# Performance work log

Hardware: AMD Instinct MI355X
Metric: run time of the kernel (lower is better)

Reference implementation:

```python
import jax, jax.numpy as jnp
import numpy as np

H = 256          # hidden_size
N_NODE = 50000   # item vocab
E_FULL = 500000  # full-graph edges
B = 1024         # sessions per batch
NODES_PER = 12   # session nodes per graph (contiguous, equal sections)
N = B * NODES_PER


def setup_inputs() -> dict:
    key = jax.random.key(0)
    ks = jax.random.split(key, 20)
    stdv = 1.0 / np.sqrt(H)
    u = lambda k, shape: jax.random.uniform(k, shape, jnp.float32, -stdv, stdv)
    return dict(
        x=jax.random.randint(ks[0], (N, 1), 1, N_NODE + 1, dtype=jnp.int32),  # 1-based item ids
        batch=jnp.repeat(jnp.arange(B, dtype=jnp.int32), NODES_PER),          # sorted graph ids
        edge_index=jax.random.randint(ks[1], (2, N), 0, N, dtype=jnp.int32),
        full_graph=jax.random.randint(ks[2], (2, E_FULL), 0, N_NODE, dtype=jnp.int32),
        emb=u(ks[3], (N_NODE, H)),
        ggnn_W=u(ks[4], (H, H)),
        gru_Wih=u(ks[5], (3 * H, H)),
        gru_Whh=u(ks[6], (3 * H, H)),
        gru_bih=u(ks[7], (3 * H,)),
        gru_bhh=u(ks[8], (3 * H,)),
        W1_w=u(ks[9], (H, H)), W1_b=u(ks[10], (H,)),
        W2_w=u(ks[11], (H, H)), W2_b=u(ks[12], (H,)),
        q_w=u(ks[13], (1, H)), q_b=u(ks[14], (1,)),
        W3_w=u(ks[15], (H, 2 * H)), W3_b=u(ks[16], (H,)),
    )


def _forward(x, batch, edge_index, full_graph, emb, ggnn_W, gru_Wih, gru_Whh,
             gru_bih, gru_bhh, W1_w, W1_b, W2_w, W2_b, q_w, q_b, W3_w, W3_b):
    # --- GatedGraphConv (num_layers=1) over the full item graph ---
    src, dst = full_graph[0], full_graph[1]
    m = emb @ ggnn_W                                      # [n_node, H]
    agg = jax.ops.segment_sum(m[src], dst, num_segments=N_NODE)  # sum aggregation
    # GRUCell(agg, emb)
    gi = agg @ gru_Wih.T + gru_bih                        # [n_node, 3H]
    gh = emb @ gru_Whh.T + gru_bhh
    i_r, i_z, i_n = jnp.split(gi, 3, axis=1)
    h_r, h_z, h_n = jnp.split(gh, 3, axis=1)
    r = jax.nn.sigmoid(i_r + h_r)
    z = jax.nn.sigmoid(i_z + h_z)
    n = jnp.tanh(i_n + r * h_n)
    hidden_all = (1.0 - z) * n + z * emb                  # [n_node, H]

    # gather session nodes (x is 1-based), relu
    h2 = jax.nn.relu(hidden_all[x[:, 0] - 1])             # [N, H]

    # --- Embedding2Score: segment attention readout ---
    sections = jax.ops.segment_sum(jnp.ones_like(batch), batch, num_segments=B)
    last_idx = jnp.cumsum(sections) - 1                   # last node of each session
    v_n = h2[last_idx]                                    # [B, H]
    v_n_rep = v_n[batch]                                  # [N, H]
    gate = jax.nn.sigmoid(v_n_rep @ W1_w.T + W1_b + h2 @ W2_w.T + W2_b)
    alpha = gate @ q_w.T + q_b                            # [N, 1]
    s_g = jax.ops.segment_sum(alpha * h2, batch, num_segments=B)  # [B, H]
    s_h = jnp.concatenate([v_n, s_g], axis=1) @ W3_w.T + W3_b     # [B, H]
    scores = s_h @ emb.T                                  # [B, n_node]
    return scores, h2


def reference(x, batch, edge_index, full_graph, emb, ggnn_W, gru_Wih, gru_Whh,
              gru_bih, gru_bhh, W1_w, W1_b, W2_w, W2_b, q_w, q_b, W3_w, W3_b):
    scores, h2 = _forward(x, batch, edge_index, full_graph, emb, ggnn_W,
                          gru_Wih, gru_Whh, gru_bih, gru_bhh,
                          W1_w, W1_b, W2_w, W2_b, q_w, q_b, W3_w, W3_b)
    return scores, h2, edge_index
```

## Files before the change

kernel.cpp:

```cpp
#include <hip/hip_runtime.h>
#include <hip/hip_bf16.h>
#include <stdint.h>

#define HDIM 256
#define NNODE 50000
#define EFULL 500000
#define BSESS 1024
#define NPER 12
#define NROWS 12288
#define CAP 96

typedef __attribute__((ext_vector_type(8))) short bf16x8;
typedef __attribute__((ext_vector_type(4))) float f32x4;
typedef __attribute__((ext_vector_type(4))) unsigned short u16x4;

__device__ __forceinline__ float bf2f(unsigned short v) {
  union { unsigned u; float f; } x; x.u = ((unsigned)v) << 16; return x.f;
}
__device__ __forceinline__ unsigned short f2bf(float f) {
  union { float f; unsigned u; } x; x.f = f;
  unsigned r = x.u + 0x7fff + ((x.u >> 16) & 1);
  return (unsigned short)(r >> 16);
}

#define CV_EMB   12800000
#define CV_GW    65536
#define CV_WIH   196608
#define CV_WHH   196608
#define CV_W1    65536
#define CV_W2    65536
#define CV_W3    131072
#define CV_BIAS  2304
#define CV_WSUM  (CV_EMB + CV_GW + CV_WIH + CV_WHH + CV_W1 + CV_W2 + CV_W3 + CV_BIAS)
#define CV_TOTAL (CV_WSUM + NNODE + 2 * NROWS)
__global__ void k_conv(const float* __restrict__ emb, const float* __restrict__ gw,
                       const float* __restrict__ wih, const float* __restrict__ whh,
                       const float* __restrict__ w1, const float* __restrict__ w2,
                       const float* __restrict__ w3,
                       const float* __restrict__ bih, const float* __restrict__ bhh,
                       const float* __restrict__ w1b, const float* __restrict__ w2b,
                       const float* __restrict__ w3b,
                       unsigned short* __restrict__ embB, unsigned short* __restrict__ gwB,
                       unsigned short* __restrict__ wihB, unsigned short* __restrict__ whhB,
                       unsigned short* __restrict__ w1B, unsigned short* __restrict__ w2B,
                       unsigned short* __restrict__ w3B, unsigned short* __restrict__ biasB,
                       int* __restrict__ map,
                       const int* __restrict__ eidx, float* __restrict__ out_e) {
  long idx = (long)blockIdx.x * 256 + threadIdx.x;
  if (idx < CV_EMB) { embB[idx] = f2bf(emb[idx]); return; }
  idx -= CV_EMB;
  if (idx < CV_GW)  { gwB[idx] = f2bf(gw[idx]); return; }
  idx -= CV_GW;
  if (idx < CV_WIH) { wihB[idx] = f2bf(wih[idx]); return; }
  idx -= CV_WIH;
  if (idx < CV_WHH) { whhB[idx] = f2bf(whh[idx]); return; }
  idx -= CV_WHH;
  if (idx < CV_W1)  { w1B[idx] = f2bf(w1[idx]); return; }
  idx -= CV_W1;
  if (idx < CV_W2)  { w2B[idx] = f2bf(w2[idx]); return; }
  idx -= CV_W2;
  if (idx < CV_W3)  { w3B[idx] = f2bf(w3[idx]); return; }
  idx -= CV_W3;
  if (idx < CV_BIAS) {
    if (idx < 768)        { biasB[idx] = f2bf(bih[idx]); return; }
    if (idx < 1536)       { biasB[idx] = f2bf(bhh[idx - 768]); return; }
    if (idx < 1792)       { biasB[idx] = f2bf(w1b[idx - 1536]); return; }
    if (idx < 2048)       { biasB[idx] = f2bf(w2b[idx - 1792]); return; }
    biasB[idx] = f2bf(w3b[idx - 2048]); return;
  }
  idx -= CV_BIAS;
  if (idx < NNODE) { map[idx] = -1; return; }
  idx -= NNODE;
  if (idx < 2 * NROWS) out_e[idx] = (float)eidx[idx];
}

__global__ void k_set_map(const int* __restrict__ x, int* __restrict__ m, int* __restrict__ cnt) {
  int i = blockIdx.x * 256 + threadIdx.x;
  if (i < NROWS) { atomicMax(&m[x[i] - 1], i); cnt[i] = 0; }
}

__global__ void k_bin(const int* __restrict__ fg, const int* __restrict__ map,
                      int* __restrict__ cnt, int* __restrict__ lists) {
  int e = blockIdx.x * 256 + threadIdx.x;
  if (e >= EFULL) return;
  int cid = map[fg[EFULL + e]];
  if (cid < 0) return;
  int pos = atomicAdd(&cnt[cid], 1);
  if (pos < CAP) lists[cid * CAP + pos] = fg[e];
}

#define PREP_COPY_BLKS 1284
#define PREP_AGG_BASE  (12 + PREP_COPY_BLKS)
__global__ __launch_bounds__(256) void k_prep(
    const unsigned short* __restrict__ WihB, const unsigned short* __restrict__ gwB,
    const unsigned short* __restrict__ WhhB,
    const float* __restrict__ bih, const float* __restrict__ bhh,
    unsigned short* __restrict__ Bbig2, unsigned short* __restrict__ bias2,
    const int* __restrict__ x, const int* __restrict__ map,
    const int* __restrict__ cnt, const int* __restrict__ lists,
    const float* __restrict__ emb, unsigned short* __restrict__ Acat) {
  __shared__ __align__(16) unsigned short As[128 * 32];
  __shared__ __align__(16) unsigned short Bs[128 * 32];
  if (blockIdx.x < 12) {
    const int bx = blockIdx.x % 6, by = blockIdx.x / 6;
    const int tid = threadIdx.x;
    const int wid = tid >> 6, lane = tid & 63;
    const int quad = lane >> 4, l15 = lane & 15;
    const int m0 = bx * 128, n0 = by * 128;
    const int wm = (wid & 1) * 64, wn = (wid >> 1) * 64;
    f32x4 acc[4][4] = {};
    const int lrow = tid >> 2;
    const int lcol = (tid & 3) * 8;
    const size_t ar0 = (size_t)(m0 + lrow) * HDIM + lcol;
    const size_t ar1 = (size_t)(m0 + lrow + 64) * HDIM + lcol;
    const size_t br0 = (size_t)(n0 + lrow) * HDIM + lcol;
    const size_t br1 = (size_t)(n0 + lrow + 64) * HDIM + lcol;
    const int ak = quad * 8;
    for (int k0 = 0; k0 < HDIM; k0 += 32) {
      *(float4*)&As[(size_t)tid * 8]        = *(const float4*)&WihB[ar0 + k0];
      *(float4*)&As[2048 + (size_t)tid * 8] = *(const float4*)&WihB[ar1 + k0];
      *(float4*)&Bs[(size_t)tid * 8]        = *(const float4*)&gwB[br0 + k0];
      *(float4*)&Bs[2048 + (size_t)tid * 8] = *(const float4*)&gwB[br1 + k0];
      __syncthreads();
      bf16x8 af[4], bfv[4];
#pragma unroll
      for (int mi = 0; mi < 4; mi++) af[mi] = *(const bf16x8*)&As[(wm + mi * 16 + l15) * 32 + ak];
#pragma unroll
      for (int ni = 0; ni < 4; ni++) bfv[ni] = *(const bf16x8*)&Bs[(wn + ni * 16 + l15) * 32 + ak];
#pragma unroll
      for (int mi = 0; mi < 4; mi++)
#pragma unroll
        for (int ni = 0; ni < 4; ni++)
          acc[mi][ni] = __builtin_amdgcn_mfma_f32_16x16x32_bf16(af[mi], bfv[ni], acc[mi][ni], 0, 0, 0);
      __syncthreads();
    }
#pragma unroll
    for (int mi = 0; mi < 4; mi++) {
      const int gr0 = m0 + wm + mi * 16 + quad * 4;
#pragma unroll
      for (int ni = 0; ni < 4; ni++) {
        const int gc = n0 + wn + ni * 16 + l15;
#pragma unroll
        for (int r = 0; r < 4; r++) {
          const int gr = gr0 + r;
          const int g = gr >> 8, c = gr & 255;
          const int jp = ((c >> 4) << 6) + (g << 4) + (c & 15);
          Bbig2[(size_t)jp * 512 + gc] = f2bf(acc[mi][ni][r]);
        }
      }
    }
    return;
  }
  if (blockIdx.x < PREP_AGG_BASE) {
    int idx = (blockIdx.x - 12) * 256 + threadIdx.x;
    if (idx < 262144) {
      int jp = idx >> 8, kk = idx & 255;
      int g = (jp >> 4) & 3, q = jp >> 6, t = jp & 15, c = q * 16 + t;
      unsigned short v = 0;
      if (g < 2)       v = WhhB[(size_t)(g * 256 + c) * HDIM + kk];
      else if (g == 3) v = WhhB[(size_t)(512 + c) * HDIM + kk];
      Bbig2[(size_t)jp * 512 + 256 + kk] = v;
      return;
    }
    idx -= 262144;
    if (idx < 65536) {
      int c = idx >> 8, k = idx & 255;
      int jp = ((c >> 4) << 6) + 48 + (c & 15);
      Bbig2[(size_t)jp * 512 + k] = 0;
      return;
    }
    idx -= 65536;
    if (idx < 1024) {
      int q = idx >> 6, g = (idx >> 4) & 3, t = idx & 15, c = q * 16 + t;
      float bv;
      if (g < 2)       bv = bih[g * 256 + c] + bhh[g * 256 + c];
      else if (g == 2) bv = bih[512 + c];
      else             bv = bhh[512 + c];
      bias2[idx] = f2bf(bv);
    }
    return;
  }
  int i = (blockIdx.x - PREP_AGG_BASE) * 4 + (threadIdx.x >> 6);
  int lane = threadIdx.x & 63;
  int node = x[i] - 1;
  int cid = map[node];
  int n = cnt[cid];
  if (n > CAP) n = CAP;
  const int* lp = lists + (size_t)cid * CAP;
  float sx = 0.f, sy = 0.f, sz = 0.f, sw = 0.f;
  int j = 0;
  for (; j + 4 <= n; j += 4) {
    int s0 = lp[j], s1 = lp[j + 1], s2 = lp[j + 2], s3 = lp[j + 3];
    float4 v0 = *(const float4*)(emb + (size_t)s0 * HDIM + lane * 4);
    float4 v1 = *(const float4*)(emb + (size_t)s1 * HDIM + lane * 4);
    float4 v2 = *(const float4*)(emb + (size_t)s2 * HDIM + lane * 4);
    float4 v3 = *(const float4*)(emb + (size_t)s3 * HDIM + lane * 4);
    sx += v0.x + v1.x + v2.x + v3.x;
    sy += v0.y + v1.y + v2.y + v3.y;
    sz += v0.z + v1.z + v2.z + v3.z;
    sw += v0.w + v1.w + v2.w + v3.w;
  }
  for (; j < n; j++) {
    int s0 = lp[j];
    float4 v0 = *(const float4*)(emb + (size_t)s0 * HDIM + lane * 4);
    sx += v0.x; sy += v0.y; sz += v0.z; sw += v0.w;
  }
  u16x4 o; o.x = f2bf(sx); o.y = f2bf(sy); o.z = f2bf(sz); o.w = f2bf(sw);
  *(u16x4*)(Acat + (size_t)i * 512 + lane * 4) = o;
  float4 v = *(const float4*)(emb + (size_t)node * HDIM + lane * 4);
  u16x4 o2; o2.x = f2bf(v.x); o2.y = f2bf(v.y); o2.z = f2bf(v.z); o2.w = f2bf(v.w);
  *(u16x4*)(Acat + (size_t)i * 512 + 256 + lane * 4) = o2;
}

template <bool OUT_BF16>
__device__ __forceinline__ void gemm128_body(
    unsigned short* As, unsigned short* Bs,
    const unsigned short* __restrict__ A, int lda,
    const unsigned short* __restrict__ Bm, int ldb,
    const unsigned short* __restrict__ bias,
    void* __restrict__ C, int ldc, int M, int N, int K, int bx, int by) {
  const int tid = threadIdx.x;
  const int wid = tid >> 6, lane = tid & 63;
  const int quad = lane >> 4, l15 = lane & 15;
  const int m0 = bx * 128, n0 = by * 128;
  const int wm = (wid & 1) * 64, wn = (wid >> 1) * 64;
  f32x4 acc[4][4] = {};
  const int lrow = tid >> 2;
  const int lcol = (tid & 3) * 8;
  const size_t ar0 = (size_t)min(m0 + lrow, M - 1) * lda + lcol;
  const size_t ar1 = (size_t)min(m0 + lrow + 64, M - 1) * lda + lcol;
  const size_t br0 = (size_t)min(n0 + lrow, N - 1) * ldb + lcol;
  const size_t br1 = (size_t)min(n0 + lrow + 64, N - 1) * ldb + lcol;
  const int ak = quad * 8;
  for (int k0 = 0; k0 < K; k0 += 32) {
    *(float4*)&As[(size_t)tid * 8]        = *(const float4*)&A[ar0 + k0];
    *(float4*)&As[2048 + (size_t)tid * 8] = *(const float4*)&A[ar1 + k0];
    *(float4*)&Bs[(size_t)tid * 8]        = *(const float4*)&Bm[br0 + k0];
    *(float4*)&Bs[2048 + (size_t)tid * 8] = *(const float4*)&Bm[br1 + k0];
    __syncthreads();
    bf16x8 af[4], bfv[4];
#pragma unroll
    for (int mi = 0; mi < 4; mi++) af[mi] = *(const bf16x8*)&As[(wm + mi * 16 + l15) * 32 + ak];
#pragma unroll
    for (int ni = 0; ni < 4; ni++) bfv[ni] = *(const bf16x8*)&Bs[(wn + ni * 16 + l15) * 32 + ak];
#pragma unroll
    for (int mi = 0; mi < 4; mi++)
#pragma unroll
      for (int ni = 0; ni < 4; ni++)
        acc[mi][ni] = __builtin_amdgcn_mfma_f32_16x16x32_bf16(af[mi], bfv[ni], acc[mi][ni], 0, 0, 0);
    __syncthreads();
  }
#pragma unroll
  for (int mi = 0; mi < 4; mi++) {
    const int gr0 = m0 + wm + mi * 16 + quad * 4;
#pragma unroll
    for (int ni = 0; ni < 4; ni++) {
      const int gc = n0 + wn + ni * 16 + l15;
      if (gc >= N) continue;
      const float bv = bias ? bf2f(bias[gc]) : 0.f;
#pragma unroll
      for (int r = 0; r < 4; r++) {
        const int gr = gr0 + r;
        if (gr < M) {
          const float v = acc[mi][ni][r] + bv;
          if (OUT_BF16) ((unsigned short*)C)[(size_t)gr * ldc + gc] = f2bf(v);
          else          ((float*)C)[(size_t)gr * ldc + gc] = v;
        }
      }
    }
  }
}

__global__ __launch_bounds__(256) void k_t12(
    const unsigned short* __restrict__ h2b, const unsigned short* __restrict__ W2, const unsigned short* __restrict__ b2,
    unsigned short* __restrict__ t2,
    const unsigned short* __restrict__ vnB, const unsigned short* __restrict__ W1, const unsigned short* __restrict__ b1,
    unsigned short* __restrict__ t1) {
  __shared__ __align__(16) unsigned short As[128 * 32];
  __shared__ __align__(16) unsigned short Bs[128 * 32];
  if (blockIdx.x < 96)
    gemm128_body<true>(As, Bs, h2b, HDIM, W2, HDIM, b2, t2, HDIM, NROWS, HDIM, HDIM, blockIdx.x, blockIdx.y);
  else
    gemm128_body<true>(As, Bs, vnB, HDIM, W1, HDIM, b1, t1, HDIM, BSESS, HDIM, HDIM, blockIdx.x - 96, blockIdx.y);
}

__global__ __launch_bounds__(512) void k_ggru(
    const unsigned short* __restrict__ Acat,
    const unsigned short* __restrict__ Bbig2,
    const unsigned short* __restrict__ bias2,
    unsigned short* __restrict__ h2b, float* __restrict__ h2out,
    unsigned short* __restrict__ vnB) {
  __shared__ __align__(16) unsigned short As[256 * 32];
  __shared__ __align__(16) unsigned short Bs[128 * 32];
  const int tid = threadIdx.x;
  const int wid = tid >> 6, lane = tid & 63;
  const int quad = lane >> 4, l15 = lane & 15;
  const int m0 = blockIdx.x * 256, n0 = blockIdx.y * 128;
  const int wm = (wid & 3) * 64, wn = (wid >> 2) * 64;
  f32x4 acc[4][4] = {};
  const int lrow = tid >> 2;
  const int lcol = (tid & 3) * 8;
  const size_t ar0 = (size_t)(m0 + lrow) * 512 + lcol;
  const size_t ar1 = (size_t)(m0 + lrow + 128) * 512 + lcol;
  const size_t br0 = (size_t)(n0 + lrow) * 512 + lcol;
  const int ak = quad * 8;
  for (int k0 = 0; k0 < 512; k0 += 32) {
    *(float4*)&As[(size_t)lrow * 32 + lcol]         = *(const float4*)&Acat[ar0 + k0];
    *(float4*)&As[(size_t)(lrow + 128) * 32 + lcol] = *(const float4*)&Acat[ar1 + k0];
    *(float4*)&Bs[(size_t)lrow * 32 + lcol]         = *(const float4*)&Bbig2[br0 + k0];
    __syncthreads();
    bf16x8 af[4], bfv[4];
#pragma unroll
    for (int mi = 0; mi < 4; mi++) af[mi] = *(const bf16x8*)&As[(wm + mi * 16 + l15) * 32 + ak];
#pragma unroll
    for (int g = 0; g < 4; g++) bfv[g] = *(const bf16x8*)&Bs[(wn + g * 16 + l15) * 32 + ak];
#pragma unroll
    for (int mi = 0; mi < 4; mi++)
#pragma unroll
      for (int g = 0; g < 4; g++)
        acc[mi][g] = __builtin_amdgcn_mfma_f32_16x16x32_bf16(af[mi], bfv[g], acc[mi][g], 0, 0, 0);
    __syncthreads();
  }
  const int ch = ((n0 + wn) >> 2) + l15;
  const float b0 = bf2f(bias2[(n0 + wn) + 0 * 16 + l15]);
  const float b1 = bf2f(bias2[(n0 + wn) + 1 * 16 + l15]);
  const float b2 = bf2f(bias2[(n0 + wn) + 2 * 16 + l15]);
  const float b3 = bf2f(bias2[(n0 + wn) + 3 * 16 + l15]);
#pragma unroll
  for (int mi = 0; mi < 4; mi++) {
    const int gr0 = m0 + wm + mi * 16 + quad * 4;
#pragma unroll
    for (int r = 0; r < 4; r++) {
      const int gr = gr0 + r;
      float rs = acc[mi][0][r] + b0;
      float zs = acc[mi][1][r] + b1;
      float inn = acc[mi][2][r] + b2;
      float hn = acc[mi][3][r] + b3;
      float rr = 1.f / (1.f + expf(-rs));
      float zz = 1.f / (1.f + expf(-zs));
      float nn = tanhf(inn + rr * hn);
      float e = bf2f(Acat[(size_t)gr * 512 + 256 + ch]);
      float h = fmaxf((1.f - zz) * nn + zz * e, 0.f);
      unsigned short hb = f2bf(h);
      h2b[(size_t)gr * HDIM + ch] = hb;
      h2out[(size_t)gr * HDIM + ch] = h;
      if (gr % NPER == NPER - 1) vnB[(size_t)(gr / NPER) * HDIM + ch] = hb;
    }
  }
}

__global__ __launch_bounds__(256) void k_attn2(
    const unsigned short* __restrict__ t1, const unsigned short* __restrict__ t2,
    const unsigned short* __restrict__ h2b,
    const float* __restrict__ qw, const float* __restrict__ qb,
    const unsigned short* __restrict__ W3, const unsigned short* __restrict__ b3,
    unsigned short* __restrict__ shb) {
  __shared__ float al[NPER];
  __shared__ float sh[512];
  const int b = blockIdx.x;
  const int w = threadIdx.x >> 6, lane = threadIdx.x & 63;
  u16x4 a = *(const u16x4*)(t1 + (size_t)b * HDIM + lane * 4);
  float4 q = *(const float4*)(qw + lane * 4);
  float ax = bf2f(a.x), ay = bf2f(a.y), az = bf2f(a.z), aw = bf2f(a.w);
#pragma unroll
  for (int i = 0; i < 3; i++) {
    int j = w * 3 + i;
    u16x4 c = *(const u16x4*)(t2 + ((size_t)b * NPER + j) * HDIM + lane * 4);
    float p = 0.f;
    p += q.x / (1.f + expf(-(ax + bf2f(c.x))));
    p += q.y / (1.f + expf(-(ay + bf2f(c.y))));
    p += q.z / (1.f + expf(-(az + bf2f(c.z))));
    p += q.w / (1.f + expf(-(aw + bf2f(c.w))));
#pragma unroll
    for (int off = 32; off > 0; off >>= 1) p += __shfl_down(p, off);
    if (lane == 0) al[j] = p + qb[0];
  }
  const int c = threadIdx.x;
  sh[c] = bf2f(h2b[((size_t)b * NPER + (NPER - 1)) * HDIM + c]);
  __syncthreads();
  float s = 0.f;
#pragma unroll
  for (int j = 0; j < NPER; j++)
    s += al[j] * bf2f(h2b[((size_t)b * NPER + j) * HDIM + c]);
  sh[256 + c] = s;
  __syncthreads();
  const unsigned short* wrow = W3 + (size_t)c * 512;
  float acc = bf2f(b3[c]);
#pragma unroll 8
  for (int k = 0; k < 512; k += 8) {
    bf16x8 wv = *(const bf16x8*)&wrow[k];
    acc += bf2f((unsigned short)wv[0]) * sh[k + 0];
    acc += bf2f((unsigned short)wv[1]) * sh[k + 1];
    acc += bf2f((unsigned short)wv[2]) * sh[k + 2];
    acc += bf2f((unsigned short)wv[3]) * sh[k + 3];
    acc += bf2f((unsigned short)wv[4]) * sh[k + 4];
    acc += bf2f((unsigned short)wv[5]) * sh[k + 5];
    acc += bf2f((unsigned short)wv[6]) * sh[k + 6];
    acc += bf2f((unsigned short)wv[7]) * sh[k + 7];
  }
  shb[(size_t)b * HDIM + c] = f2bf(acc);
}

template <bool OUT_BF16>
__global__ __launch_bounds__(512) void k_gemm_nt2(
    const unsigned short* __restrict__ A, int lda,
    const unsigned short* __restrict__ Bm, int ldb,
    const unsigned short* __restrict__ bias,
    void* __restrict__ C, int ldc, int M, int N, int K) {
  __shared__ __align__(16) unsigned short As[256 * 32];
  __shared__ __align__(16) unsigned short Bs[128 * 32];
  const int tid = threadIdx.x;
  const int wid = tid >> 6, lane = tid & 63;
  const int quad = lane >> 4, l15 = lane & 15;
  const int m0 = blockIdx.x * 256, n0 = blockIdx.y * 128;
  const int wm = (wid & 3) * 64, wn = (wid >> 2) * 64;
  f32x4 acc[4][4] = {};
  const int lrow = tid >> 2;
  const int lcol = (tid & 3) * 8;
  const size_t ar0 = (size_t)min(m0 + lrow, M - 1) * lda + lcol;
  const size_t ar1 = (size_t)min(m0 + lrow + 128, M - 1) * lda + lcol;
  const size_t br0 = (size_t)min(n0 + lrow, N - 1) * ldb + lcol;
  const int ak = quad * 8;
  for (int k0 = 0; k0 < K; k0 += 32) {
    *(float4*)&As[(size_t)lrow * 32 + lcol]         = *(const float4*)&A[ar0 + k0];
    *(float4*)&As[(size_t)(lrow + 128) * 32 + lcol] = *(const float4*)&A[ar1 + k0];
    *(float4*)&Bs[(size_t)lrow * 32 + lcol]         = *(const float4*)&Bm[br0 + k0];
    __syncthreads();
    bf16x8 af[4], bfv[4];
#pragma unroll
    for (int mi = 0; mi < 4; mi++) af[mi] = *(const bf16x8*)&As[(wm + mi * 16 + l15) * 32 + ak];
#pragma unroll
    for (int ni = 0; ni < 4; ni++) bfv[ni] = *(const bf16x8*)&Bs[(wn + ni * 16 + l15) * 32 + ak];
#pragma unroll
    for (int mi = 0; mi < 4; mi++)
#pragma unroll
      for (int ni = 0; ni < 4; ni++)
        acc[mi][ni] = __builtin_amdgcn_mfma_f32_16x16x32_bf16(af[mi], bfv[ni], acc[mi][ni], 0, 0, 0);
    __syncthreads();
  }
#pragma unroll
  for (int mi = 0; mi < 4; mi++) {
    const int gr0 = m0 + wm + mi * 16 + quad * 4;
#pragma unroll
    for (int ni = 0; ni < 4; ni++) {
      const int gc = n0 + wn + ni * 16 + l15;
      if (gc >= N) continue;
      const float bv = bias ? bf2f(bias[gc]) : 0.f;
#pragma unroll
      for (int r = 0; r < 4; r++) {
        const int gr = gr0 + r;
        if (gr < M) {
          const float v = acc[mi][ni][r] + bv;
          if (OUT_BF16) ((unsigned short*)C)[(size_t)gr * ldc + gc] = f2bf(v);
          else          ((float*)C)[(size_t)gr * ldc + gc] = v;
        }
      }
    }
  }
}

extern "C" void kernel_launch(void* const* d_in, const int* in_sizes, int n_in,
                              void* d_out, int out_size, void* d_ws, size_t ws_size,
                              hipStream_t stream) {
  const int* x     = (const int*)d_in[0];
  const int* batch = (const int*)d_in[1];
  const int* eidx  = (const int*)d_in[2];
  const int* fg    = (const int*)d_in[3];
  const float* emb   = (const float*)d_in[4];
  const float* ggnnW = (const float*)d_in[5];
  const float* Wih   = (const float*)d_in[6];
  const float* Whh   = (const float*)d_in[7];
  const float* bih   = (const float*)d_in[8];
  const float* bhh   = (const float*)d_in[9];
  const float* W1w   = (const float*)d_in[10];
  const float* W1b   = (const float*)d_in[11];
  const float* W2w   = (const float*)d_in[12];
  const float* W2b   = (const float*)d_in[13];
  const float* qw    = (const float*)d_in[14];
  const float* qb    = (const float*)d_in[15];
  const float* W3w   = (const float*)d_in[16];
  const float* W3b   = (const float*)d_in[17];
  (void)batch;

  char* w = (char*)d_ws;
  size_t off = 0;
  auto alloc = [&](size_t bytes) { char* p = w + off; off += (bytes + 511) & ~(size_t)511; return p; };
  int*            map   = (int*)alloc((size_t)NNODE * 4);
  int*            cnt   = (int*)alloc((size_t)NROWS * 4);
  int*            lists = (int*)alloc((size_t)NROWS * CAP * 4);
  unsigned short* Acat  = (unsigned short*)alloc((size_t)NROWS * 512 * 2);
  unsigned short* embB  = (unsigned short*)alloc((size_t)NNODE * HDIM * 2);
  unsigned short* gwB   = (unsigned short*)alloc((size_t)CV_GW * 2);
  unsigned short* WihB  = (unsigned short*)alloc((size_t)CV_WIH * 2);
  unsigned short* WhhB  = (unsigned short*)alloc((size_t)CV_WHH * 2);
  unsigned short* W1wB  = (unsigned short*)alloc((size_t)CV_W1 * 2);
  unsigned short* W2wB  = (unsigned short*)alloc((size_t)CV_W2 * 2);
  unsigned short* W3wB  = (unsigned short*)alloc((size_t)CV_W3 * 2);
  unsigned short* biasB = (unsigned short*)alloc((size_t)CV_BIAS * 2);
  unsigned short* Bbig2 = (unsigned short*)alloc((size_t)1024 * 512 * 2);
  unsigned short* bias2 = (unsigned short*)alloc((size_t)1024 * 2);
  unsigned short* h2b   = (unsigned short*)alloc((size_t)NROWS * HDIM * 2);
  unsigned short* vnB   = (unsigned short*)alloc((size_t)BSESS * HDIM * 2);
  unsigned short* t1    = (unsigned short*)alloc((size_t)BSESS * HDIM * 2);
  unsigned short* t2    = (unsigned short*)alloc((size_t)NROWS * HDIM * 2);
  unsigned short* shb   = (unsigned short*)alloc((size_t)BSESS * HDIM * 2);
  if (off > ws_size) return;

  float* out_scores = (float*)d_out;
  float* out_h2     = out_scores + (size_t)BSESS * NNODE;
  float* out_e      = out_h2 + (size_t)NROWS * HDIM;

  dim3 blk(256);
  k_conv   <<<(CV_TOTAL + 255) / 256, blk, 0, stream>>>(emb, ggnnW, Wih, Whh, W1w, W2w, W3w,
               bih, bhh, W1b, W2b, W3b, embB, gwB, WihB, WhhB, W1wB, W2wB, W3wB, biasB,
               map, eidx, out_e);
  k_set_map<<<(NROWS + 255) / 256, blk, 0, stream>>>(x, map, cnt);
  k_bin    <<<(EFULL + 255) / 256, blk, 0, stream>>>(fg, map, cnt, lists);
  k_prep   <<<PREP_AGG_BASE + NROWS / 4, blk, 0, stream>>>(WihB, gwB, WhhB, bih, bhh, Bbig2, bias2,
               x, map, cnt, lists, emb, Acat);
  k_ggru   <<<dim3(48, 8), dim3(512), 0, stream>>>(Acat, Bbig2, bias2, h2b, out_h2, vnB);
  k_t12    <<<dim3(104, 2), blk, 0, stream>>>(h2b, W2wB, biasB + 1792, t2, vnB, W1wB, biasB + 1536, t1);
  k_attn2  <<<BSESS, blk, 0, stream>>>(t1, t2, h2b, qw, qb, W3wB, biasB + 2048, shb);
  k_gemm_nt2<false><<<dim3(4, 391), dim3(512), 0, stream>>>(shb, HDIM, embB, HDIM, nullptr, out_scores, NNODE, BSESS, NNODE, HDIM);
}
```

Measured before the change: 476.5 us.

## Fuse emb bf16 conversion into scores GEMM and shrink GGRU tiles

Removes the separate full-table fp32-to-bf16 conversion of the embedding matrix (12.8M elements) from k_conv and converts emb tiles on the fly inside a specialized scores GEMM kernel. This drops one write and one read of a bf16 copy of emb, but the scores kernel now reads fp32 emb (twice the bytes per tile) and converts it redundantly across the 4 row-block tiles. Separately, the GGRU GEMM moves from 256x128 tiles with 512 threads to 128x128 tiles with 256 threads, doubling the block count for better occupancy and balance.

```diff
diff --git a/kernel.cpp b/kernel.cpp
--- a/kernel.cpp
+++ b/kernel.cpp
@@ -23,7 +23,6 @@
   return (unsigned short)(r >> 16);
 }
 
-#define CV_EMB   12800000
 #define CV_GW    65536
 #define CV_WIH   196608
 #define CV_WHH   196608
@@ -31,24 +30,22 @@
 #define CV_W2    65536
 #define CV_W3    131072
 #define CV_BIAS  2304
-#define CV_WSUM  (CV_EMB + CV_GW + CV_WIH + CV_WHH + CV_W1 + CV_W2 + CV_W3 + CV_BIAS)
+#define CV_WSUM  (CV_GW + CV_WIH + CV_WHH + CV_W1 + CV_W2 + CV_W3 + CV_BIAS)
 #define CV_TOTAL (CV_WSUM + NNODE + 2 * NROWS)
-__global__ void k_conv(const float* __restrict__ emb, const float* __restrict__ gw,
+__global__ void k_conv(const float* __restrict__ gw,
                        const float* __restrict__ wih, const float* __restrict__ whh,
                        const float* __restrict__ w1, const float* __restrict__ w2,
                        const float* __restrict__ w3,
                        const float* __restrict__ bih, const float* __restrict__ bhh,
                        const float* __restrict__ w1b, const float* __restrict__ w2b,
                        const float* __restrict__ w3b,
-                       unsigned short* __restrict__ embB, unsigned short* __restrict__ gwB,
+                       unsigned short* __restrict__ gwB,
                        unsigned short* __restrict__ wihB, unsigned short* __restrict__ whhB,
                        unsigned short* __restrict__ w1B, unsigned short* __restrict__ w2B,
                        unsigned short* __restrict__ w3B, unsigned short* __restrict__ biasB,
                        int* __restrict__ map,
                        const int* __restrict__ eidx, float* __restrict__ out_e) {
   long idx = (long)blockIdx.x * 256 + threadIdx.x;
-  if (idx < CV_EMB) { embB[idx] = f2bf(emb[idx]); return; }
-  idx -= CV_EMB;
   if (idx < CV_GW)  { gwB[idx] = f2bf(gw[idx]); return; }
   idx -= CV_GW;
   if (idx < CV_WIH) { wihB[idx] = f2bf(wih[idx]); return; }
@@ -284,30 +281,32 @@
     gemm128_body<true>(As, Bs, vnB, HDIM, W1, HDIM, b1, t1, HDIM, BSESS, HDIM, HDIM, blockIdx.x - 96, blockIdx.y);
 }
 
-__global__ __launch_bounds__(512) void k_ggru(
+__global__ __launch_bounds__(256) void k_ggru(
     const unsigned short* __restrict__ Acat,
     const unsigned short* __restrict__ Bbig2,
     const unsigned short* __restrict__ bias2,
     unsigned short* __restrict__ h2b, float* __restrict__ h2out,
     unsigned short* __restrict__ vnB) {
-  __shared__ __align__(16) unsigned short As[256 * 32];
+  __shared__ __align__(16) unsigned short As[128 * 32];
   __shared__ __align__(16) unsigned short Bs[128 * 32];
   const int tid = threadIdx.x;
   const int wid = tid >> 6, lane = tid & 63;
   const int quad = lane >> 4, l15 = lane & 15;
-  const int m0 = blockIdx.x * 256, n0 = blockIdx.y * 128;
-  const int wm = (wid & 3) * 64, wn = (wid >> 2) * 64;
+  const int m0 = blockIdx.x * 128, n0 = blockIdx.y * 128;
+  const int wm = (wid & 1) * 64, wn = (wid >> 1) * 64;
   f32x4 acc[4][4] = {};
   const int lrow = tid >> 2;
   const int lcol = (tid & 3) * 8;
   const size_t ar0 = (size_t)(m0 + lrow) * 512 + lcol;
-  const size_t ar1 = (size_t)(m0 + lrow + 128) * 512 + lcol;
+  const size_t ar1 = (size_t)(m0 + lrow + 64) * 512 + lcol;
   const size_t br0 = (size_t)(n0 + lrow) * 512 + lcol;
+  const size_t br1 = (size_t)(n0 + lrow + 64) * 512 + lcol;
   const int ak = quad * 8;
   for (int k0 = 0; k0 < 512; k0 += 32) {
-    *(float4*)&As[(size_t)lrow * 32 + lcol]         = *(const float4*)&Acat[ar0 + k0];
-    *(float4*)&As[(size_t)(lrow + 128) * 32 + lcol] = *(const float4*)&Acat[ar1 + k0];
-    *(float4*)&Bs[(size_t)lrow * 32 + lcol]         = *(const float4*)&Bbig2[br0 + k0];
+    *(float4*)&As[(size_t)tid * 8]        = *(const float4*)&Acat[ar0 + k0];
+    *(float4*)&As[2048 + (size_t)tid * 8] = *(const float4*)&Acat[ar1 + k0];
+    *(float4*)&Bs[(size_t)tid * 8]        = *(const float4*)&Bbig2[br0 + k0];
+    *(float4*)&Bs[2048 + (size_t)tid * 8] = *(const float4*)&Bbig2[br1 + k0];
     __syncthreads();
     bf16x8 af[4], bfv[4];
 #pragma unroll
@@ -401,12 +400,10 @@
   shb[(size_t)b * HDIM + c] = f2bf(acc);
 }
 
-template <bool OUT_BF16>
-__global__ __launch_bounds__(512) void k_gemm_nt2(
-    const unsigned short* __restrict__ A, int lda,
-    const unsigned short* __restrict__ Bm, int ldb,
-    const unsigned short* __restrict__ bias,
-    void* __restrict__ C, int ldc, int M, int N, int K) {
+__global__ __launch_bounds__(512) void k_scores(
+    const unsigned short* __restrict__ A,
+    const float* __restrict__ Bf,
+    float* __restrict__ C) {
   __shared__ __align__(16) unsigned short As[256 * 32];
   __shared__ __align__(16) unsigned short Bs[128 * 32];
   const int tid = threadIdx.x;
@@ -417,14 +414,21 @@
   f32x4 acc[4][4] = {};
   const int lrow = tid >> 2;
   const int lcol = (tid & 3) * 8;
-  const size_t ar0 = (size_t)min(m0 + lrow, M - 1) * lda + lcol;
-  const size_t ar1 = (size_t)min(m0 + lrow + 128, M - 1) * lda + lcol;
-  const size_t br0 = (size_t)min(n0 + lrow, N - 1) * ldb + lcol;
+  const size_t ar0 = (size_t)min(m0 + lrow, BSESS - 1) * HDIM + lcol;
+  const size_t ar1 = (size_t)min(m0 + lrow + 128, BSESS - 1) * HDIM + lcol;
+  const size_t br0 = (size_t)min(n0 + lrow, NNODE - 1) * HDIM + lcol;
   const int ak = quad * 8;
-  for (int k0 = 0; k0 < K; k0 += 32) {
+  for (int k0 = 0; k0 < HDIM; k0 += 32) {
     *(float4*)&As[(size_t)lrow * 32 + lcol]         = *(const float4*)&A[ar0 + k0];
     *(float4*)&As[(size_t)(lrow + 128) * 32 + lcol] = *(const float4*)&A[ar1 + k0];
-    *(float4*)&Bs[(size_t)lrow * 32 + lcol]         = *(const float4*)&Bm[br0 + k0];
+    float4 f0 = *(const float4*)&Bf[br0 + k0];
+    float4 f1 = *(const float4*)&Bf[br0 + k0 + 4];
+    bf16x8 bv;
+    bv[0] = (short)f2bf(f0.x); bv[1] = (short)f2bf(f0.y);
+    bv[2] = (short)f2bf(f0.z); bv[3] = (short)f2bf(f0.w);
+    bv[4] = (short)f2bf(f1.x); bv[5] = (short)f2bf(f1.y);
+    bv[6] = (short)f2bf(f1.z); bv[7] = (short)f2bf(f1.w);
+    *(bf16x8*)&Bs[(size_t)lrow * 32 + lcol] = bv;
     __syncthreads();
     bf16x8 af[4], bfv[4];
 #pragma unroll
@@ -444,16 +448,11 @@
 #pragma unroll
     for (int ni = 0; ni < 4; ni++) {
       const int gc = n0 + wn + ni * 16 + l15;
-      if (gc >= N) continue;
-      const float bv = bias ? bf2f(bias[gc]) : 0.f;
+      if (gc >= NNODE) continue;
 #pragma unroll
       for (int r = 0; r < 4; r++) {
         const int gr = gr0 + r;
-        if (gr < M) {
-          const float v = acc[mi][ni][r] + bv;
-          if (OUT_BF16) ((unsigned short*)C)[(size_t)gr * ldc + gc] = f2bf(v);
-          else          ((float*)C)[(size_t)gr * ldc + gc] = v;
-        }
+        C[(size_t)gr * NNODE + gc] = acc[mi][ni][r];
       }
     }
   }
@@ -489,7 +488,6 @@
   int*            cnt   = (int*)alloc((size_t)NROWS * 4);
   int*            lists = (int*)alloc((size_t)NROWS * CAP * 4);
   unsigned short* Acat  = (unsigned short*)alloc((size_t)NROWS * 512 * 2);
-  unsigned short* embB  = (unsigned short*)alloc((size_t)NNODE * HDIM * 2);
   unsigned short* gwB   = (unsigned short*)alloc((size_t)CV_GW * 2);
   unsigned short* WihB  = (unsigned short*)alloc((size_t)CV_WIH * 2);
   unsigned short* WhhB  = (unsigned short*)alloc((size_t)CV_WHH * 2);
@@ -511,15 +509,15 @@
   float* out_e      = out_h2 + (size_t)NROWS * HDIM;
 
   dim3 blk(256);
-  k_conv   <<<(CV_TOTAL + 255) / 256, blk, 0, stream>>>(emb, ggnnW, Wih, Whh, W1w, W2w, W3w,
-               bih, bhh, W1b, W2b, W3b, embB, gwB, WihB, WhhB, W1wB, W2wB, W3wB, biasB,
+  k_conv   <<<(CV_TOTAL + 255) / 256, blk, 0, stream>>>(ggnnW, Wih, Whh, W1w, W2w, W3w,
+               bih, bhh, W1b, W2b, W3b, gwB, WihB, WhhB, W1wB, W2wB, W3wB, biasB,
                map, eidx, out_e);
   k_set_map<<<(NROWS + 255) / 256, blk, 0, stream>>>(x, map, cnt);
   k_bin    <<<(EFULL + 255) / 256, blk, 0, stream>>>(fg, map, cnt, lists);
   k_prep   <<<PREP_AGG_BASE + NROWS / 4, blk, 0, stream>>>(WihB, gwB, WhhB, bih, bhh, Bbig2, bias2,
                x, map, cnt, lists, emb, Acat);
-  k_ggru   <<<dim3(48, 8), dim3(512), 0, stream>>>(Acat, Bbig2, bias2, h2b, out_h2, vnB);
+  k_ggru   <<<dim3(96, 8), blk, 0, stream>>>(Acat, Bbig2, bias2, h2b, out_h2, vnB);
   k_t12    <<<dim3(104, 2), blk, 0, stream>>>(h2b, W2wB, biasB + 1792, t2, vnB, W1wB, biasB + 1536, t1);
   k_attn2  <<<BSESS, blk, 0, stream>>>(t1, t2, h2b, qw, qb, W3wB, biasB + 2048, shb);
-  k_gemm_nt2<false><<<dim3(4, 391), dim3(512), 0, stream>>>(shb, HDIM, embB, HDIM, nullptr, out_scores, NNODE, BSESS, NNODE, HDIM);
-}
+  k_scores <<<dim3(4, 391), dim3(512), 0, stream>>>(shb, emb, out_scores);
+}
```

Result: faster. 463.4 us (-2.8%).
